# Kernel optimization log

Measured on AMD Instinct MI355X. Metric: run time of the kernel, lower is better.

## Reference

```python
import jax, jax.numpy as jnp
import numpy as np

EPS = 1e-8


def quaternion_mul(q, m):
    # Hamilton product q * m over last dim of size 4 (w, x, y, z)
    w1, x1, y1, z1 = q[..., 0], q[..., 1], q[..., 2], q[..., 3]
    w2, x2, y2, z2 = m[..., 0], m[..., 1], m[..., 2], m[..., 3]
    return jnp.stack([
        w1 * w2 - x1 * x2 - y1 * y2 - z1 * z2,
        w1 * x2 + x1 * w2 + y1 * z2 - z1 * y2,
        w1 * y2 - x1 * z2 + y1 * w2 + z1 * x2,
        w1 * z2 + x1 * y2 - y1 * x2 + z1 * w2,
    ], axis=-1)


def quaternion_normalize(q):
    n = jnp.linalg.norm(q, axis=-1, keepdims=True)
    return q / (n + EPS)


def setup_inputs() -> dict:
    key = jax.random.key(0)
    k = jax.random.split(key, 5)
    B, S, D, H = 4, 2048, 1024, 1024
    scale = 0.02
    return {
        "x": jax.random.normal(k[0], (B, S, D), dtype=jnp.float32),
        "W_in": jax.random.normal(k[1], (3 * H, D), dtype=jnp.float32) * scale,
        "b_in": jax.random.normal(k[2], (3 * H,), dtype=jnp.float32) * scale,
        "W_out": jax.random.normal(k[3], (D, 4 * H), dtype=jnp.float32) * scale,
        "b_out": jax.random.normal(k[4], (D,), dtype=jnp.float32) * scale,
    }


def reference(x, W_in, b_in, W_out, b_out):
    B, S, D = x.shape
    H = W_in.shape[0] // 3
    # input projection -> rotation parameters v in R^3 per hidden channel
    v = (jnp.einsum('bsd,ed->bse', x, W_in) + b_in).reshape(B, S, H, 3)
    # SU(2) exponential map: v -> unit quaternion
    theta = jnp.linalg.norm(v, axis=-1, keepdims=True)          # (B,S,H,1)
    axis = v / (theta + EPS)
    q_inputs = jnp.concatenate([jnp.cos(theta), jnp.sin(theta) * axis], axis=-1)  # (B,S,H,4)

    # initial identity quaternion state (B,H,4)
    m0 = jnp.zeros((B, H, 4), dtype=x.dtype).at[..., 0].set(1.0)

    def step(m, q_t):
        m_new = quaternion_normalize(quaternion_mul(q_t, m))
        return m_new, m_new

    q_seq = jnp.transpose(q_inputs, (1, 0, 2, 3))               # (S,B,H,4)
    m_final, ms = jax.lax.scan(step, m0, q_seq)                 # ms: (S,B,H,4)

    states = jnp.transpose(ms, (1, 0, 2, 3)).reshape(B, S, 4 * H)
    full_output = jnp.einsum('bsf,df->bsd', states, W_out) + b_out
    return full_output, m_final
```

## Files before the change

kernel.cpp:

```cpp
#include <hip/hip_runtime.h>
#include <hip/hip_bf16.h>
#include <stdint.h>

#define EPSF 1e-8f

typedef __attribute__((ext_vector_type(8))) short short8;
typedef __attribute__((ext_vector_type(8))) _Float16 half8;
typedef __attribute__((ext_vector_type(4))) float floatx4;

__device__ __forceinline__ unsigned short f2h(float f) {
    _Float16 h = (_Float16)f;
    return __builtin_bit_cast(unsigned short, h);
}
__device__ __forceinline__ float h2f(unsigned short u) {
    return (float)__builtin_bit_cast(_Float16, u);
}


__global__ void prep_kernel(const float4* __restrict__ x4, ushort4* __restrict__ x16,
                            const float4* __restrict__ wi4, ushort4* __restrict__ wi16,
                            const float4* __restrict__ wo4, ushort4* __restrict__ wo16,
                            int nx4, int nw4, int nwo4) {
    int i = blockIdx.x * blockDim.x + threadIdx.x;
    float4 f; ushort4 u;
    if (i < nx4) {
        f = x4[i];
        u.x = f2h(f.x); u.y = f2h(f.y); u.z = f2h(f.z); u.w = f2h(f.w);
        x16[i] = u;
    } else if (i < nx4 + nw4) {
        int j = i - nx4;
        f = wi4[j];
        u.x = f2h(f.x); u.y = f2h(f.y); u.z = f2h(f.z); u.w = f2h(f.w);
        wi16[j] = u;
    } else if (i < nx4 + nw4 + nwo4) {
        int j = i - nx4 - nw4;
        f = wo4[j];
        u.x = f2h(f.x); u.y = f2h(f.y); u.z = f2h(f.z); u.w = f2h(f.w);
        wo16[j] = u;
    }
}


__device__ __forceinline__ void gld16(const unsigned short* g, unsigned short* l) {
    __builtin_amdgcn_global_load_lds(
        (const __attribute__((address_space(1))) unsigned int*)g,
        (__attribute__((address_space(3))) unsigned int*)l, 16, 0, 0);
}

template <bool HALFOUT>
__global__ __launch_bounds__(512, 2)
void gemm8p(const unsigned short* __restrict__ Am, const unsigned short* __restrict__ Bm,
            const float* __restrict__ bias, void* __restrict__ Cv,
            int M, int N, int K) {
    constexpr int BM = 256, BN = 128, BK = 64;
    constexpr int ASZ  = BM * BK;
    constexpr int BSZ  = BN * BK;
    constexpr int SLOT = ASZ + BSZ;
    extern __shared__ unsigned short smem[];

    const int tid  = threadIdx.x;
    const int lane = tid & 63;
    const int wid  = tid >> 6;
    const int wr   = wid >> 1;
    const int wc   = wid & 1;
    const int q4   = lane >> 4;
    const int m16  = lane & 15;
    const int x7   = m16 & 7;

    const int nbx = N / BN;
    const int nwg = gridDim.x;
    const int q   = nwg >> 3;
    const int wg  = blockIdx.x;
    const int sz  = (wg & 7) * q + (wg >> 3);
    const int bx  = sz % nbx, by = sz / nbx;
    const int rowA0 = by * BM, rowB0 = bx * BN;

    const int rA = tid >> 3, cA = tid & 7;
    const int cg = cA ^ (rA & 7);
    const unsigned short* srcA = Am + (size_t)(rowA0 + rA) * K + cg * 8;
    const unsigned short* srcB = Bm + (size_t)(rowB0 + rA) * K + cg * 8;
    const int dA = tid * 8;

    int aoffm[4], boffn[4];
#pragma unroll
    for (int m = 0; m < 4; ++m) aoffm[m] = (wr * 64 + m * 16 + m16) * BK;
#pragma unroll
    for (int n = 0; n < 4; ++n) boffn[n] = (wc * 64 + n * 16 + m16) * BK;

    floatx4 acc[4][4];
#pragma unroll
    for (int m = 0; m < 4; ++m)
#pragma unroll
        for (int n = 0; n < 4; ++n)
#pragma unroll
            for (int r = 0; r < 4; ++r) acc[m][n][r] = 0.f;

    const int NT = K / BK;

    auto stageA = [&](int s, int t, int j) {
        gld16(srcA + (size_t)(j * 64) * K + (size_t)t * BK,
              smem + s * SLOT + j * 4096 + dA);
    };
    auto stageB = [&](int s, int t, int j) {
        gld16(srcB + (size_t)(j * 64) * K + (size_t)t * BK,
              smem + s * SLOT + ASZ + j * 4096 + dA);
    };

    auto RD = [&](const unsigned short* tA, const unsigned short* tB, int kh,
                  short8* Ra, short8* Rb) {
        const int xo = ((kh * 4 + q4) ^ x7) * 8;
#pragma unroll
        for (int m = 0; m < 4; ++m) Ra[m] = *(const short8*)(tA + aoffm[m] + xo);
#pragma unroll
        for (int n = 0; n < 4; ++n) Rb[n] = *(const short8*)(tB + boffn[n] + xo);
    };
    auto MM = [&](short8* Ra, short8* Rb) {
        __builtin_amdgcn_s_setprio(1);
#pragma unroll
        for (int m = 0; m < 4; ++m)
#pragma unroll
            for (int n = 0; n < 4; ++n)
                acc[m][n] = __builtin_amdgcn_mfma_f32_16x16x32_f16(
                    __builtin_bit_cast(half8, Ra[m]), __builtin_bit_cast(half8, Rb[n]),
                    acc[m][n], 0, 0, 0);
        __builtin_amdgcn_s_setprio(0);
    };

#pragma unroll
    for (int j = 0; j < 4; ++j) stageA(0, 0, j);
    stageB(0, 0, 0); stageB(0, 0, 1);
#pragma unroll
    for (int j = 0; j < 4; ++j) stageA(1, 1, j);
    stageB(1, 1, 0); stageB(1, 1, 1);

    asm volatile("s_waitcnt vmcnt(6)" ::: "memory");
    __builtin_amdgcn_s_barrier();
    __builtin_amdgcn_sched_barrier(0);

    short8 RA0[4], RB0[4], RA1[4], RB1[4];
    RD(smem, smem + ASZ, 0, RA0, RB0);

    int s0 = 0;
    for (int t = 0; t < NT; ++t) {
        __builtin_amdgcn_s_barrier();
        __builtin_amdgcn_sched_barrier(0);

        int s1 = s0 + 1; if (s1 == 3) s1 = 0;
        int s2 = s1 + 1; if (s2 == 3) s2 = 0;
        const unsigned short* tA  = smem + s0 * SLOT;
        const unsigned short* tB  = tA + ASZ;
        const unsigned short* tA1 = smem + s1 * SLOT;
        const unsigned short* tB1 = tA1 + ASZ;

        if (t + 2 < NT) {
#pragma unroll
            for (int j = 0; j < 4; ++j) stageA(s2, t + 2, j);
            stageB(s2, t + 2, 0); stageB(s2, t + 2, 1);
        }

        RD(tA, tB, 1, RA1, RB1);
        MM(RA0, RB0);

        if (t + 2 < NT) asm volatile("s_waitcnt vmcnt(6)" ::: "memory");
        else            asm volatile("s_waitcnt vmcnt(0)" ::: "memory");
        __builtin_amdgcn_s_barrier();
        __builtin_amdgcn_sched_barrier(0);

        if (t + 1 < NT) RD(tA1, tB1, 0, RA0, RB0);
        MM(RA1, RB1);

        s0 = s1;
    }

#pragma unroll
    for (int m = 0; m < 4; ++m) {
#pragma unroll
        for (int n = 0; n < 4; ++n) {
            int col  = rowB0 + wc * 64 + n * 16 + m16;
            float bvl = bias[col];
#pragma unroll
            for (int r = 0; r < 4; ++r) {
                int row = rowA0 + wr * 64 + m * 16 + q4 * 4 + r;
                if (HALFOUT)
                    ((unsigned short*)Cv)[(size_t)row * N + col] = f2h(acc[m][n][r] + bvl);
                else
                    ((float*)Cv)[(size_t)row * N + col] = acc[m][n][r] + bvl;
            }
        }
    }
}


struct Q { float w, x, y, z; };

__device__ __forceinline__ Q qmul(Q a, Q b) {
    Q r;
    r.w = a.w * b.w - a.x * b.x - a.y * b.y - a.z * b.z;
    r.x = a.w * b.x + a.x * b.w + a.y * b.z - a.z * b.y;
    r.y = a.w * b.y - a.x * b.z + a.y * b.w + a.z * b.x;
    r.z = a.w * b.z + a.x * b.y - a.y * b.x + a.z * b.w;
    return r;
}
__device__ __forceinline__ Q qnorm(Q a) {
    float nn = a.w * a.w + a.x * a.x + a.y * a.y + a.z * a.z;
    float inv = __frsqrt_rn(nn);
    Q r; r.w = a.w * inv; r.x = a.x * inv; r.y = a.y * inv; r.z = a.z * inv;
    return r;
}
__device__ __forceinline__ Q vquat(float vx, float vy, float vz) {
    float th = sqrtf(vx * vx + vy * vy + vz * vz);
    float s_, c_;
    __sincosf(th, &s_, &c_);
    float k = __fdividef(s_, th + EPSF);
    Q q; q.w = c_; q.x = k * vx; q.y = k * vy; q.z = k * vz;
    return q;
}

#define SEG  64
#define NSEG 32

__global__ __launch_bounds__(256)
void seg_prod_kernel(const unsigned short* __restrict__ v, float* __restrict__ partials,
                     int S, int H) {
    const int b  = blockIdx.z;
    const int h  = blockIdx.y * 64 + (threadIdx.x & 63);
    const int sg = blockIdx.x * 4 + (threadIdx.x >> 6);
    const int s0 = sg * SEG;
    const size_t vstep = (size_t)3 * H;
    const unsigned short* vp = v + ((size_t)b * S + s0) * vstep + (size_t)h * 3;

    constexpr int CH = 8;
    float ax[CH], ay[CH], az[CH], bx[CH], by[CH], bz[CH];
#pragma unroll
    for (int i = 0; i < CH; ++i) {
        ax[i] = h2f(vp[i * vstep + 0]); ay[i] = h2f(vp[i * vstep + 1]); az[i] = h2f(vp[i * vstep + 2]);
    }
    Q c = {1.f, 0.f, 0.f, 0.f};
    const int NC = SEG / CH;
    for (int cc = 0; cc < NC; cc += 2) {
        if (cc + 1 < NC) {
            const unsigned short* p = vp + (size_t)(cc + 1) * CH * vstep;
#pragma unroll
            for (int i = 0; i < CH; ++i) {
                bx[i] = h2f(p[i * vstep + 0]); by[i] = h2f(p[i * vstep + 1]); bz[i] = h2f(p[i * vstep + 2]);
            }
        }
#pragma unroll
        for (int i = 0; i < CH; ++i) c = qmul(vquat(ax[i], ay[i], az[i]), c);
        if (cc + 2 < NC) {
            const unsigned short* p = vp + (size_t)(cc + 2) * CH * vstep;
#pragma unroll
            for (int i = 0; i < CH; ++i) {
                ax[i] = h2f(p[i * vstep + 0]); ay[i] = h2f(p[i * vstep + 1]); az[i] = h2f(p[i * vstep + 2]);
            }
        }
#pragma unroll
        for (int i = 0; i < CH; ++i) c = qmul(vquat(bx[i], by[i], bz[i]), c);
    }
    float4* dst = (float4*)(partials + (((size_t)b * NSEG + sg) * H + h) * 4);
    *dst = make_float4(c.w, c.x, c.y, c.z);
}

__global__ __launch_bounds__(256)
void apply_kernel(const unsigned short* __restrict__ v, const float* __restrict__ partials,
                  unsigned short* __restrict__ st, float* __restrict__ m_final,
                  int S, int H) {
    const int b   = blockIdx.z;
    const int hb  = blockIdx.y * 64;
    const int hl  = threadIdx.x & 63;
    const int h   = hb + hl;
    const int sg  = blockIdx.x * 4 + (threadIdx.x >> 6);
    const int s0  = sg * SEG;
    const size_t vstep = (size_t)3 * H;
    const size_t sstep = (size_t)4 * H;
    const unsigned short* vp = v + ((size_t)b * S + s0) * vstep + (size_t)h * 3;
    unsigned short* sp = st + ((size_t)b * S + s0) * sstep + (size_t)h * 4;

    __shared__ float4 lp[NSEG][64];
    for (int i = threadIdx.x; i < NSEG * 64; i += 256) {
        int s2 = i >> 6, hh = i & 63;
        lp[s2][hh] = *(const float4*)(partials + (((size_t)b * NSEG + s2) * H + hb + hh) * 4);
    }
    __syncthreads();

    Q R = {1.f, 0.f, 0.f, 0.f};
    for (int s2 = 0; s2 < sg; ++s2) {
        float4 pv = lp[s2][hl];
        Q pq = {pv.x, pv.y, pv.z, pv.w};
        R = qmul(pq, R);
    }

    constexpr int CH = 8;
    float ax[CH], ay[CH], az[CH], bx[CH], by[CH], bz[CH];
#pragma unroll
    for (int i = 0; i < CH; ++i) {
        ax[i] = h2f(vp[i * vstep + 0]); ay[i] = h2f(vp[i * vstep + 1]); az[i] = h2f(vp[i * vstep + 2]);
    }
    const int NC = SEG / CH;
    for (int cc = 0; cc < NC; cc += 2) {
        if (cc + 1 < NC) {
            const unsigned short* pp = vp + (size_t)(cc + 1) * CH * vstep;
#pragma unroll
            for (int i = 0; i < CH; ++i) {
                bx[i] = h2f(pp[i * vstep + 0]); by[i] = h2f(pp[i * vstep + 1]); bz[i] = h2f(pp[i * vstep + 2]);
            }
        }
#pragma unroll
        for (int i = 0; i < CH; ++i) {
            R = qmul(vquat(ax[i], ay[i], az[i]), R);
            Q m = qnorm(R);
            ushort4 u; u.x = f2h(m.w); u.y = f2h(m.x); u.z = f2h(m.y); u.w = f2h(m.z);
            *(ushort4*)(sp + (size_t)(cc * CH + i) * sstep) = u;
        }
        if (cc + 2 < NC) {
            const unsigned short* pp = vp + (size_t)(cc + 2) * CH * vstep;
#pragma unroll
            for (int i = 0; i < CH; ++i) {
                ax[i] = h2f(pp[i * vstep + 0]); ay[i] = h2f(pp[i * vstep + 1]); az[i] = h2f(pp[i * vstep + 2]);
            }
        }
#pragma unroll
        for (int i = 0; i < CH; ++i) {
            R = qmul(vquat(bx[i], by[i], bz[i]), R);
            Q m = qnorm(R);
            ushort4 u; u.x = f2h(m.w); u.y = f2h(m.x); u.z = f2h(m.y); u.w = f2h(m.z);
            *(ushort4*)(sp + (size_t)((cc + 1) * CH + i) * sstep) = u;
        }
    }

    if (sg == NSEG - 1) {
        Q m = qnorm(R);
        float* mf = m_final + ((size_t)b * H + h) * 4;
        mf[0] = m.w; mf[1] = m.x; mf[2] = m.y; mf[3] = m.z;
    }
}


extern "C" void kernel_launch(void* const* d_in, const int* in_sizes, int n_in,
                              void* d_out, int out_size, void* d_ws, size_t ws_size,
                              hipStream_t stream) {
    const float* x     = (const float*)d_in[0];
    const float* W_in  = (const float*)d_in[1];
    const float* b_in  = (const float*)d_in[2];
    const float* W_out = (const float*)d_in[3];
    const float* b_out = (const float*)d_in[4];
    float* out = (float*)d_out;

    const int B = 4, S = 2048, D = 1024, H = 1024;
    const int M  = B * S;
    const int N1 = 3 * H;
    const int K1 = D;
    const int N2 = D;
    const int K2 = 4 * H;

    char* ws = (char*)d_ws;
    unsigned short* v    = (unsigned short*)(ws);
    unsigned short* st   = (unsigned short*)(ws + 50331648u);
    unsigned short* x16  = (unsigned short*)(ws + 50331648u);
    unsigned short* wi16 = (unsigned short*)(ws + 50331648u + 16777216u);
    unsigned short* wo16 = (unsigned short*)(ws + 117440512u);

    float* partials = out;

    const int nx  = M * K1;
    const int nw  = N1 * K1;
    const int nwo = N2 * K2;
    const int n4  = (nx + nw + nwo) / 4;

    constexpr int LDSB = 147456;
    static int attr_done = 0;
    if (!attr_done) {
        hipFuncSetAttribute(reinterpret_cast<const void*>(&gemm8p<true>),
                            hipFuncAttributeMaxDynamicSharedMemorySize, LDSB);
        hipFuncSetAttribute(reinterpret_cast<const void*>(&gemm8p<false>),
                            hipFuncAttributeMaxDynamicSharedMemorySize, LDSB);
        attr_done = 1;
    }

    prep_kernel<<<(n4 + 255) / 256, 256, 0, stream>>>(
        (const float4*)x, (ushort4*)x16, (const float4*)W_in, (ushort4*)wi16,
        (const float4*)W_out, (ushort4*)wo16, nx / 4, nw / 4, nwo / 4);

    gemm8p<true><<<dim3((M / 256) * (N1 / 128)), 512, LDSB, stream>>>(
        x16, wi16, b_in, v, M, N1, K1);

    dim3 sg_grid(NSEG / 4, H / 64, B);
    seg_prod_kernel<<<sg_grid, 256, 0, stream>>>(v, partials, S, H);
    apply_kernel<<<sg_grid, 256, 0, stream>>>(v, partials, st, out + (size_t)M * D, S, H);

    gemm8p<false><<<dim3((M / 256) * (N2 / 128)), 512, LDSB, stream>>>(
        st, wo16, b_out, out, M, N2, K2);
}
```

Before: 303.0 us.

## Use 256x256-tile split-K GEMM with atomic accumulation for output projection

```diff
diff --git a/kernel.cpp b/kernel.cpp
--- a/kernel.cpp
+++ b/kernel.cpp
@@ -40,12 +40,12 @@
     }
 }
 
-
 __device__ __forceinline__ void gld16(const unsigned short* g, unsigned short* l) {
     __builtin_amdgcn_global_load_lds(
         (const __attribute__((address_space(1))) unsigned int*)g,
         (__attribute__((address_space(3))) unsigned int*)l, 16, 0, 0);
 }
+
 
 template <bool HALFOUT>
 __global__ __launch_bounds__(512, 2)
@@ -61,8 +61,7 @@
     const int tid  = threadIdx.x;
     const int lane = tid & 63;
     const int wid  = tid >> 6;
-    const int wr   = wid >> 1;
-    const int wc   = wid & 1;
+    const int wr   = wid >> 1, wc = wid & 1;
     const int q4   = lane >> 4;
     const int m16  = lane & 15;
     const int x7   = m16 & 7;
@@ -105,7 +104,6 @@
         gld16(srcB + (size_t)(j * 64) * K + (size_t)t * BK,
               smem + s * SLOT + ASZ + j * 4096 + dA);
     };
-
     auto RD = [&](const unsigned short* tA, const unsigned short* tB, int kh,
                   short8* Ra, short8* Rb) {
         const int xo = ((kh * 4 + q4) ^ x7) * 8;
@@ -185,6 +183,160 @@
                     ((unsigned short*)Cv)[(size_t)row * N + col] = f2h(acc[m][n][r] + bvl);
                 else
                     ((float*)Cv)[(size_t)row * N + col] = acc[m][n][r] + bvl;
+            }
+        }
+    }
+}
+
+
+__global__ __launch_bounds__(512, 2)
+void gemm256(const unsigned short* __restrict__ Am, const unsigned short* __restrict__ Bm,
+             const float* __restrict__ bias, float* __restrict__ C,
+             int M, int N, int K, int KS) {
+    constexpr int BM = 256, BN = 256, BK = 64;
+    constexpr int ASZ  = BM * BK;
+    constexpr int SLOT = (BM + BN) * BK;
+    extern __shared__ unsigned short smem[];
+
+    const int tid  = threadIdx.x;
+    const int lane = tid & 63;
+    const int wid  = tid >> 6;
+    const int wr   = wid >> 2;
+    const int wc   = wid & 3;
+    const int q4   = lane >> 4;
+    const int m16  = lane & 15;
+
+    const int nwg = gridDim.x;
+    const int qq  = nwg >> 3;
+    const int wg  = blockIdx.x;
+    const int sz  = (wg & 7) * qq + (wg >> 3);
+    const int ks  = sz >> 7;
+    const int rm  = sz & 127;
+    const int by  = rm >> 2, bx = rm & 3;
+    const int rowA0 = by * BM, rowB0 = bx * BN;
+    const int k0 = ks * KS;
+
+    const int rS = tid >> 3, cS = tid & 7;
+    const int cg = cS ^ (rS & 7);
+    const unsigned short* srcA = Am + (size_t)(rowA0 + rS) * K + k0 + cg * 8;
+    const unsigned short* srcB = Bm + (size_t)(rowB0 + rS) * K + k0 + cg * 8;
+    const int dA = tid * 8;
+
+    auto stA = [&](int s, int t, int j) {
+        gld16(srcA + (size_t)(j * 64) * K + (size_t)t * BK,
+              smem + s * SLOT + j * 4096 + dA);
+    };
+    auto stB = [&](int s, int t, int j) {
+        gld16(srcB + (size_t)(j * 64) * K + (size_t)t * BK,
+              smem + s * SLOT + ASZ + j * 4096 + dA);
+    };
+
+    int arow[8], brow[4];
+#pragma unroll
+    for (int i = 0; i < 8; ++i) arow[i] = wr * 128 + i * 16 + m16;
+#pragma unroll
+    for (int i = 0; i < 4; ++i) brow[i] = wc * 64 + i * 16 + m16;
+
+    floatx4 acc[8][4];
+#pragma unroll
+    for (int m = 0; m < 8; ++m)
+#pragma unroll
+        for (int n = 0; n < 4; ++n)
+#pragma unroll
+            for (int r = 0; r < 4; ++r) acc[m][n][r] = 0.f;
+
+    short8 Af[4][2];
+    short8 Bf[2][2][2];
+
+    auto RDA = [&](const unsigned short* base, int mh) {
+#pragma unroll
+        for (int i = 0; i < 4; ++i) {
+            int rr = arow[mh * 4 + i];
+#pragma unroll
+            for (int k = 0; k < 2; ++k)
+                Af[i][k] = *(const short8*)(base + rr * 64 + (((k * 4 + q4) ^ (rr & 7)) * 8));
+        }
+    };
+    auto RDB = [&](const unsigned short* base, int nh) {
+#pragma unroll
+        for (int i = 0; i < 2; ++i) {
+            int rr = brow[nh * 2 + i];
+#pragma unroll
+            for (int k = 0; k < 2; ++k)
+                Bf[nh][i][k] = *(const short8*)(base + ASZ + rr * 64 + (((k * 4 + q4) ^ (rr & 7)) * 8));
+        }
+    };
+    auto MMp = [&](int mh, int nh) {
+        __builtin_amdgcn_s_setprio(1);
+#pragma unroll
+        for (int i = 0; i < 4; ++i)
+#pragma unroll
+            for (int j = 0; j < 2; ++j)
+#pragma unroll
+                for (int k = 0; k < 2; ++k)
+                    acc[mh * 4 + i][nh * 2 + j] = __builtin_amdgcn_mfma_f32_16x16x32_f16(
+                        __builtin_bit_cast(half8, Af[i][k]),
+                        __builtin_bit_cast(half8, Bf[nh][j][k]),
+                        acc[mh * 4 + i][nh * 2 + j], 0, 0, 0);
+        __builtin_amdgcn_s_setprio(0);
+    };
+
+    const int NT = KS / BK;
+
+#pragma unroll
+    for (int j = 0; j < 4; ++j) stA(0, 0, j);
+#pragma unroll
+    for (int j = 0; j < 4; ++j) stB(0, 0, j);
+
+    int s0 = 0;
+    for (int t = 0; t < NT; ++t) {
+        asm volatile("s_waitcnt vmcnt(0)" ::: "memory");
+        __builtin_amdgcn_s_barrier();
+        __builtin_amdgcn_sched_barrier(0);
+
+        const unsigned short* base = smem + s0 * SLOT;
+        const int s1 = s0 ^ 1;
+        const bool pf = (t + 1 < NT);
+
+        RDA(base, 0); RDB(base, 0);
+        if (pf) { stA(s1, t + 1, 0); stA(s1, t + 1, 1); }
+        __builtin_amdgcn_s_barrier();
+        asm volatile("s_waitcnt lgkmcnt(0)" ::: "memory");
+        __builtin_amdgcn_sched_barrier(0);
+        MMp(0, 0);
+        __builtin_amdgcn_s_barrier();
+
+        RDB(base, 1);
+        if (pf) { stA(s1, t + 1, 2); stA(s1, t + 1, 3); stB(s1, t + 1, 0); }
+        __builtin_amdgcn_s_barrier();
+        asm volatile("s_waitcnt lgkmcnt(0)" ::: "memory");
+        __builtin_amdgcn_sched_barrier(0);
+        MMp(0, 1);
+        __builtin_amdgcn_s_barrier();
+
+        RDA(base, 1);
+        if (pf) { stB(s1, t + 1, 1); stB(s1, t + 1, 2); stB(s1, t + 1, 3); }
+        __builtin_amdgcn_s_barrier();
+        asm volatile("s_waitcnt lgkmcnt(0)" ::: "memory");
+        __builtin_amdgcn_sched_barrier(0);
+        MMp(1, 1);
+        __builtin_amdgcn_s_barrier();
+
+        MMp(1, 0);
+
+        s0 = s1;
+    }
+
+#pragma unroll
+    for (int m = 0; m < 8; ++m) {
+#pragma unroll
+        for (int n = 0; n < 4; ++n) {
+            int col = rowB0 + wc * 64 + n * 16 + m16;
+            float bvl = (ks == 0) ? bias[col] : 0.f;
+#pragma unroll
+            for (int r = 0; r < 4; ++r) {
+                int row = rowA0 + wr * 128 + m * 16 + q4 * 4 + r;
+                atomicAdd(&C[(size_t)row * N + col], acc[m][n][r] + bvl);
             }
         }
     }
@@ -367,13 +519,14 @@
     const int nwo = N2 * K2;
     const int n4  = (nx + nw + nwo) / 4;
 
-    constexpr int LDSB = 147456;
+    constexpr int LDSB1 = 147456;
+    constexpr int LDSB2 = 131072;
     static int attr_done = 0;
     if (!attr_done) {
         hipFuncSetAttribute(reinterpret_cast<const void*>(&gemm8p<true>),
-                            hipFuncAttributeMaxDynamicSharedMemorySize, LDSB);
-        hipFuncSetAttribute(reinterpret_cast<const void*>(&gemm8p<false>),
-                            hipFuncAttributeMaxDynamicSharedMemorySize, LDSB);
+                            hipFuncAttributeMaxDynamicSharedMemorySize, LDSB1);
+        hipFuncSetAttribute(reinterpret_cast<const void*>(&gemm256),
+                            hipFuncAttributeMaxDynamicSharedMemorySize, LDSB2);
         attr_done = 1;
     }
 
@@ -381,13 +534,14 @@
         (const float4*)x, (ushort4*)x16, (const float4*)W_in, (ushort4*)wi16,
         (const float4*)W_out, (ushort4*)wo16, nx / 4, nw / 4, nwo / 4);
 
-    gemm8p<true><<<dim3((M / 256) * (N1 / 128)), 512, LDSB, stream>>>(
+    gemm8p<true><<<dim3((M / 256) * (N1 / 128)), 512, LDSB1, stream>>>(
         x16, wi16, b_in, v, M, N1, K1);
 
     dim3 sg_grid(NSEG / 4, H / 64, B);
     seg_prod_kernel<<<sg_grid, 256, 0, stream>>>(v, partials, S, H);
     apply_kernel<<<sg_grid, 256, 0, stream>>>(v, partials, st, out + (size_t)M * D, S, H);
 
-    gemm8p<false><<<dim3((M / 256) * (N2 / 128)), 512, LDSB, stream>>>(
-        st, wo16, b_out, out, M, N2, K2);
-}
+    hipMemsetAsync(out, 0, (size_t)M * D * sizeof(float), stream);
+    gemm256<<<dim3(32 * 4 * 2), 512, LDSB2, stream>>>(
+        st, wo16, b_out, out, M, N2, K2, K2 / 2);
+}
```

After: 333.1 us. 9.9% more time.
